# Kernel tuning notes

Measured on AMD Instinct MI355X. Metric: run time of the kernel, lower is better.

Reference implementation:

```python
import jax, jax.numpy as jnp
import numpy as np

D_MODEL = 1024
N_HEADS = 16
HEAD_DIM = D_MODEL // N_HEADS


def setup_inputs() -> dict:
    key = jax.random.key(0)
    ks = jax.random.split(key, 12)
    B, S = 1, 4096
    s = 1.0 / np.sqrt(D_MODEL)
    return {
        "query": jax.random.normal(ks[0], (B, S, D_MODEL), jnp.float32),
        "key": jax.random.normal(ks[1], (B, S, D_MODEL), jnp.float32),
        "value": jax.random.normal(ks[2], (B, S, D_MODEL), jnp.float32),
        "attention_mask": jnp.ones((B, S), jnp.int32),
        "Wq": jax.random.normal(ks[3], (D_MODEL, D_MODEL), jnp.float32) * s,
        "bq": jax.random.normal(ks[4], (D_MODEL,), jnp.float32) * s,
        "Wk": jax.random.normal(ks[5], (D_MODEL, D_MODEL), jnp.float32) * s,
        "bk": jax.random.normal(ks[6], (D_MODEL,), jnp.float32) * s,
        "Wv": jax.random.normal(ks[7], (D_MODEL, D_MODEL), jnp.float32) * s,
        "bv": jax.random.normal(ks[8], (D_MODEL,), jnp.float32) * s,
        "Wo": jax.random.normal(ks[9], (D_MODEL, D_MODEL), jnp.float32) * s,
        "bo": jax.random.normal(ks[10], (D_MODEL,), jnp.float32) * s,
    }


def reference(query, key, value, attention_mask, Wq, bq, Wk, bk, Wv, bv, Wo, bo):
    B = query.shape[0]

    def split_heads(x):  # [B,S,D] -> [B,H,S,Dh]
        return x.reshape(B, -1, N_HEADS, HEAD_DIM).transpose(0, 2, 1, 3)

    q = split_heads(query @ Wq + bq)
    k = split_heads(key @ Wk + bk)
    v = split_heads(value @ Wv + bv)

    scores = jnp.einsum("bhqd,bhkd->bhqk", q, k) / np.sqrt(HEAD_DIM)
    # 2D mask [B, Skv] -> [B,1,1,Skv]; 0 positions filled with -1e9
    mask = attention_mask[:, None, None, :]
    scores = jnp.where(mask == 0, jnp.float32(-1e9), scores)
    weights = jax.nn.softmax(scores, axis=-1)
    out = jnp.einsum("bhqk,bhkd->bhqd", weights, v)
    out = out.transpose(0, 2, 1, 3).reshape(B, -1, D_MODEL)
    return out @ Wo + bo
```

## Files before the change

### kernel.cpp

```cpp
#include <hip/hip_runtime.h>
#include <hip/hip_bf16.h>
#include <cstdint>

typedef __attribute__((ext_vector_type(8))) short short8;
typedef __attribute__((ext_vector_type(4))) float floatx4;
typedef unsigned short u16;

#define D_MODEL 1024
#define S_LEN 4096
#define N_HEADS 16
#define HEAD_DIM 64
#define SCALE_LOG2E 0.18033688f

__device__ __forceinline__ u16 f2bf(float x) {
    union { float f; uint32_t u; } v; v.f = x;
    uint32_t u = v.u;
    u += 0x7fffu + ((u >> 16) & 1u);
    return (u16)(u >> 16);
}

__device__ __forceinline__ void load_lds16(const u16* g, u16* l) {
    __builtin_amdgcn_global_load_lds(
        (const __attribute__((address_space(1))) uint32_t*)g,
        (__attribute__((address_space(3))) uint32_t*)l, 16, 0, 0);
}

#define PREP_CONV 12288
#define PREP_TR   4096
struct PrepArgs {
    const float* cs[3]; u16* cd[3];
    const float* ts[4]; u16* td[4]; float tscale[4];
    const int* mask; float* madd; int* clean;
};
__global__ __launch_bounds__(256) void prep(PrepArgs a) {
    __shared__ u16 tile[32][34];
    const int bx = blockIdx.x;
    const int tid = threadIdx.x;
    if (bx < PREP_CONV) {
        const int z = bx >> 12;
        const int i = (bx & 4095) * 256 + tid;
        float4 v = reinterpret_cast<const float4*>(a.cs[z])[i];
        ushort4 o;
        o.x = f2bf(v.x); o.y = f2bf(v.y); o.z = f2bf(v.z); o.w = f2bf(v.w);
        reinterpret_cast<ushort4*>(a.cd[z])[i] = o;
    } else if (bx < PREP_CONV + PREP_TR) {
        const int b = bx - PREP_CONV;
        const int z = b >> 10;
        const int t = b & 1023;
        const float* __restrict__ in = a.ts[z];
        u16* __restrict__ out = a.td[z];
        const float sc = a.tscale[z];
        const int c0 = (t & 31) * 32, r0 = (t >> 5) * 32;
        const int tx = tid & 31, ty = tid >> 5;
        #pragma unroll
        for (int j = 0; j < 32; j += 8)
            tile[ty + j][tx] = f2bf(in[(size_t)(r0 + ty + j) * D_MODEL + c0 + tx] * sc);
        __syncthreads();
        #pragma unroll
        for (int j = 0; j < 32; j += 8)
            out[(size_t)(c0 + ty + j) * D_MODEL + r0 + tx] = tile[tx][ty + j];
    } else {
        const int b = bx - PREP_CONV - PREP_TR;
        const int i = b * 256 + tid;
        const int v = a.mask[i];
        a.madd[i] = (v == 0) ? -1.0e30f : 0.f;
        const unsigned long long bal = __ballot(v != 0);
        if ((tid & 63) == 0) a.clean[b * 4 + (tid >> 6)] = (bal == ~0ull) ? 1 : 0;
    }
}

template <typename OutT>
__device__ __forceinline__ void gemm_bt_core(const u16* __restrict__ A, const u16* __restrict__ Bt,
                                             const float* __restrict__ bias, OutT* __restrict__ C,
                                             int M, int N, int K, int bx, int by, int trC,
                                             float bscale) {
    __shared__ u16 As[3][128 * 64];
    __shared__ u16 Bs[3][128 * 64];
    const int tid = threadIdx.x;
    const int wave = tid >> 6, lane = tid & 63;
    const int quad = lane >> 4, n16 = lane & 15;
    const int wm = wave >> 1, wn = wave & 1;
    const int m0 = by * 128, n0 = bx * 128;
    const int rl = lane >> 3, cl = lane & 7;
    const int stg_c = (cl ^ (rl & 7)) * 8;
    const int swz = n16 & 7;
    const int KI = K >> 6;

    floatx4 acc[4][4];
    #pragma unroll
    for (int i = 0; i < 4; ++i)
        #pragma unroll
        for (int t = 0; t < 4; ++t) acc[i][t] = (floatx4)0.f;

    #pragma unroll
    for (int p = 0; p < 2; ++p) {
        #pragma unroll
        for (int u = 0; u < 4; ++u) {
            const int r = wave * 32 + u * 8 + rl;
            load_lds16(&A[(size_t)(m0 + r) * K + p * 64 + stg_c], &As[p][(wave * 32 + u * 8) * 64]);
            load_lds16(&Bt[(size_t)(n0 + r) * K + p * 64 + stg_c], &Bs[p][(wave * 32 + u * 8) * 64]);
        }
    }

    int cur = 0;
    #pragma unroll 1
    for (int it = 0; it < KI; ++it) {
        asm volatile("s_waitcnt vmcnt(8)\n\ts_barrier" ::: "memory");
        const int nb = (cur >= 1) ? cur - 1 : 2;
        const int kn = ((it + 2) & (KI - 1)) * 64;
        #pragma unroll
        for (int u = 0; u < 4; ++u) {
            const int r = wave * 32 + u * 8 + rl;
            load_lds16(&A[(size_t)(m0 + r) * K + kn + stg_c], &As[nb][(wave * 32 + u * 8) * 64]);
            load_lds16(&Bt[(size_t)(n0 + r) * K + kn + stg_c], &Bs[nb][(wave * 32 + u * 8) * 64]);
        }
        #pragma unroll
        for (int kk = 0; kk < 2; ++kk) {
            const int sw = ((kk * 4 + quad) ^ swz) * 8;
            short8 a[4], b[4];
            #pragma unroll
            for (int i = 0; i < 4; ++i)
                a[i] = *reinterpret_cast<const short8*>(&As[cur][(wm * 64 + i * 16 + n16) * 64 + sw]);
            #pragma unroll
            for (int t = 0; t < 4; ++t)
                b[t] = *reinterpret_cast<const short8*>(&Bs[cur][(wn * 64 + t * 16 + n16) * 64 + sw]);
            #pragma unroll
            for (int i = 0; i < 4; ++i)
                #pragma unroll
                for (int t = 0; t < 4; ++t)
                    acc[i][t] = __builtin_amdgcn_mfma_f32_16x16x32_bf16(a[i], b[t], acc[i][t], 0, 0, 0);
        }
        cur = (cur >= 2) ? 0 : cur + 1;
    }
    asm volatile("s_waitcnt vmcnt(0)" ::: "memory");

    if (trC) {
        if constexpr (sizeof(OutT) == 2) {
            #pragma unroll
            for (int t = 0; t < 4; ++t) {
                const int col = n0 + wn * 64 + t * 16 + n16;
                const float bvs = bias[col] * bscale;
                #pragma unroll
                for (int i = 0; i < 4; ++i) {
                    const int row = m0 + wm * 64 + i * 16 + quad * 4;
                    ushort4 o;
                    o.x = f2bf(acc[i][t][0] + bvs);
                    o.y = f2bf(acc[i][t][1] + bvs);
                    o.z = f2bf(acc[i][t][2] + bvs);
                    o.w = f2bf(acc[i][t][3] + bvs);
                    *reinterpret_cast<ushort4*>(&C[(size_t)col * M + row]) = o;
                }
            }
        }
    } else {
        #pragma unroll
        for (int t = 0; t < 4; ++t) {
            const int col = n0 + wn * 64 + t * 16 + n16;
            const float bvs = bias[col] * bscale;
            #pragma unroll
            for (int i = 0; i < 4; ++i) {
                #pragma unroll
                for (int r = 0; r < 4; ++r) {
                    const int row = m0 + wm * 64 + i * 16 + quad * 4 + r;
                    const float val = acc[i][t][r] + bvs;
                    if constexpr (sizeof(OutT) == 2) C[(size_t)row * N + col] = f2bf(val);
                    else                             C[(size_t)row * N + col] = val;
                }
            }
        }
    }
}

struct QkvArgs {
    const u16* A[3]; const u16* B[3]; const float* bias[3]; u16* C[3]; float bscale[3];
};

__global__ __launch_bounds__(256) void gemm_qkv(QkvArgs args, int M, int N, int K) {
    const int z = blockIdx.z;
    gemm_bt_core<u16>(args.A[z], args.B[z], args.bias[z], args.C[z], M, N, K,
                      blockIdx.x, blockIdx.y, z == 2 ? 1 : 0, args.bscale[z]);
}

__global__ __launch_bounds__(256) void gemm_out(const u16* __restrict__ A, const u16* __restrict__ Bt,
                                                const float* __restrict__ bias, float* __restrict__ C,
                                                int M, int N, int K) {
    gemm_bt_core<float>(A, Bt, bias, C, M, N, K, blockIdx.x, blockIdx.y, 0, 1.0f);
}

__global__ __launch_bounds__(512) void flash_attn(const u16* __restrict__ Q, const u16* __restrict__ Kb,
                                                  const u16* __restrict__ Vt,
                                                  const float* __restrict__ madd,
                                                  const int* __restrict__ clean,
                                                  u16* __restrict__ O) {
    __shared__ u16 Ks[3 * 64 * 64];
    __shared__ u16 Vs[3 * 64 * 64];
    __shared__ u16 Ps[8][16 * 64];
    const int tid = threadIdx.x;
    const int wave = tid >> 6, lane = tid & 63;
    const int quad = lane >> 4, n16 = lane & 15;
    const int bid = blockIdx.x;
    const int h = (bid & 7) * 2 + ((bid >> 3) & 1);
    const int qt = bid >> 4;
    const int hd = h * HEAD_DIM;
    const int q0 = qt * 128 + wave * 16;

    const int rl = lane >> 3, cl = lane & 7;
    const int swz = n16 & 7;
    const int stg_row = wave * 8 + rl;
    const int stg_c = (cl ^ (rl & 7)) * 8;
    const int ldst = (wave * 8) * 64;

    short8 b_q[2];
    #pragma unroll
    for (int kk = 0; kk < 2; ++kk)
        b_q[kk] = *reinterpret_cast<const short8*>(
            &Q[(size_t)(q0 + n16) * D_MODEL + hd + kk * 32 + quad * 8]);

    short8 vone;
    #pragma unroll
    for (int i = 0; i < 8; ++i) vone[i] = (short)0x3F80;

    floatx4 o_acc[4];
    floatx4 l_acc = (floatx4)0.f;
    #pragma unroll
    for (int t = 0; t < 4; ++t) o_acc[t] = (floatx4)0.f;

    #pragma unroll
    for (int p = 0; p < 2; ++p) {
        load_lds16(&Kb[(size_t)(p * 64 + stg_row) * D_MODEL + hd + stg_c], &Ks[p * 4096 + ldst]);
        load_lds16(&Vt[(size_t)(hd + stg_row) * S_LEN + p * 64 + stg_c], &Vs[p * 4096 + ldst]);
    }

    int cur = 0;
    #pragma unroll 1
    for (int it = 0; it < 64; ++it) {
        asm volatile("s_waitcnt vmcnt(2)\n\ts_barrier" ::: "memory");

        const int nb = (cur >= 1) ? cur - 1 : 2;
        const int kn = ((it + 2) & 63) * 64;
        load_lds16(&Kb[(size_t)(kn + stg_row) * D_MODEL + hd + stg_c], &Ks[nb * 4096 + ldst]);
        load_lds16(&Vt[(size_t)(hd + stg_row) * S_LEN + kn + stg_c], &Vs[nb * 4096 + ldst]);

        const u16* KsC = &Ks[cur * 4096];
        const u16* VsC = &Vs[cur * 4096];

        floatx4 s[4];
        #pragma unroll
        for (int t = 0; t < 4; ++t) {
            s[t] = (floatx4)0.f;
            #pragma unroll
            for (int kk = 0; kk < 2; ++kk) {
                const int sw = ((kk * 4 + quad) ^ swz) * 8;
                short8 ak = *reinterpret_cast<const short8*>(&KsC[(t * 16 + n16) * 64 + sw]);
                s[t] = __builtin_amdgcn_mfma_f32_16x16x32_bf16(ak, b_q[kk], s[t], 0, 0, 0);
            }
        }
        if (clean[it]) {
            #pragma unroll
            for (int t = 0; t < 4; ++t) {
                const float p0 = __builtin_amdgcn_exp2f(s[t][0]);
                const float p1 = __builtin_amdgcn_exp2f(s[t][1]);
                const float p2 = __builtin_amdgcn_exp2f(s[t][2]);
                const float p3 = __builtin_amdgcn_exp2f(s[t][3]);
                union { __hip_bfloat162 h; uint32_t u; } pa, pb;
                pa.h = __float22bfloat162_rn(make_float2(p0, p1));
                pb.h = __float22bfloat162_rn(make_float2(p2, p3));
                uint2 w; w.x = pa.u; w.y = pb.u;
                const int cw = t * 2 + (quad >> 1);
                *reinterpret_cast<uint2*>(
                    &Ps[wave][n16 * 64 + ((cw ^ swz) * 8 + (quad & 1) * 4)]) = w;
            }
        } else {
            const int k0 = it * 64;
            #pragma unroll
            for (int t = 0; t < 4; ++t) {
                const float4 mv = *reinterpret_cast<const float4*>(&madd[k0 + t * 16 + quad * 4]);
                const float p0 = __builtin_amdgcn_exp2f(s[t][0] + mv.x);
                const float p1 = __builtin_amdgcn_exp2f(s[t][1] + mv.y);
                const float p2 = __builtin_amdgcn_exp2f(s[t][2] + mv.z);
                const float p3 = __builtin_amdgcn_exp2f(s[t][3] + mv.w);
                union { __hip_bfloat162 h; uint32_t u; } pa, pb;
                pa.h = __float22bfloat162_rn(make_float2(p0, p1));
                pb.h = __float22bfloat162_rn(make_float2(p2, p3));
                uint2 w; w.x = pa.u; w.y = pb.u;
                const int cw = t * 2 + (quad >> 1);
                *reinterpret_cast<uint2*>(
                    &Ps[wave][n16 * 64 + ((cw ^ swz) * 8 + (quad & 1) * 4)]) = w;
            }
        }
        asm volatile("s_waitcnt lgkmcnt(0)" ::: "memory");
        short8 ap[2];
        #pragma unroll
        for (int kkv = 0; kkv < 2; ++kkv)
            ap[kkv] = *reinterpret_cast<const short8*>(
                &Ps[wave][n16 * 64 + ((kkv * 4 + quad) ^ swz) * 8]);
        asm volatile("" ::: "memory");
        #pragma unroll
        for (int kkv = 0; kkv < 2; ++kkv) {
            l_acc = __builtin_amdgcn_mfma_f32_16x16x32_bf16(ap[kkv], vone, l_acc, 0, 0, 0);
            #pragma unroll
            for (int t = 0; t < 4; ++t) {
                const int sw = ((kkv * 4 + quad) ^ swz) * 8;
                short8 bv = *reinterpret_cast<const short8*>(&VsC[(t * 16 + n16) * 64 + sw]);
                o_acc[t] = __builtin_amdgcn_mfma_f32_16x16x32_bf16(ap[kkv], bv, o_acc[t], 0, 0, 0);
            }
        }
        cur = (cur >= 2) ? 0 : cur + 1;
    }
    asm volatile("s_waitcnt vmcnt(0)" ::: "memory");
    float lir[4];
    #pragma unroll
    for (int r = 0; r < 4; ++r) lir[r] = 1.f / l_acc[r];
    #pragma unroll
    for (int t = 0; t < 4; ++t)
        #pragma unroll
        for (int r = 0; r < 4; ++r)
            O[(size_t)(q0 + quad * 4 + r) * D_MODEL + hd + t * 16 + n16] =
                f2bf(o_acc[t][r] * lir[r]);
}

extern "C" void kernel_launch(void* const* d_in, const int* in_sizes, int n_in,
                              void* d_out, int out_size, void* d_ws, size_t ws_size,
                              hipStream_t stream) {
    const float* query = (const float*)d_in[0];
    const float* key   = (const float*)d_in[1];
    const float* value = (const float*)d_in[2];
    const int*   mask  = (const int*)d_in[3];
    const float* Wq = (const float*)d_in[4];
    const float* bq = (const float*)d_in[5];
    const float* Wk = (const float*)d_in[6];
    const float* bk = (const float*)d_in[7];
    const float* Wv = (const float*)d_in[8];
    const float* bv = (const float*)d_in[9];
    const float* Wo = (const float*)d_in[10];
    const float* bo = (const float*)d_in[11];
    float* out = (float*)d_out;

    char* ws = (char*)d_ws;
    const size_t SZ_SD = (size_t)S_LEN * D_MODEL * 2;
    const size_t SZ_W  = (size_t)D_MODEL * D_MODEL * 2;
    u16* qb  = (u16*)(ws);
    u16* kb  = (u16*)(ws + SZ_SD);
    u16* vb  = (u16*)(ws + 2 * SZ_SD);
    u16* Wqt = (u16*)(ws + 3 * SZ_SD);
    u16* Wkt = (u16*)(ws + 3 * SZ_SD + SZ_W);
    u16* Wvt = (u16*)(ws + 3 * SZ_SD + 2 * SZ_W);
    u16* Wot = (u16*)(ws + 3 * SZ_SD + 3 * SZ_W);
    u16* Qp  = (u16*)(ws + 3 * SZ_SD + 4 * SZ_W);
    u16* Kp  = (u16*)(ws + 4 * SZ_SD + 4 * SZ_W);
    u16* Vpt = (u16*)(ws + 5 * SZ_SD + 4 * SZ_W);
    float* maddf = (float*)(ws + 6 * SZ_SD + 4 * SZ_W);
    int* cleanf  = (int*)(ws + 6 * SZ_SD + 4 * SZ_W + S_LEN * sizeof(float));
    u16* Oa  = kb;

    PrepArgs pa;
    pa.cs[0] = query; pa.cs[1] = key; pa.cs[2] = value;
    pa.cd[0] = qb;    pa.cd[1] = kb;  pa.cd[2] = vb;
    pa.ts[0] = Wq; pa.ts[1] = Wk; pa.ts[2] = Wv; pa.ts[3] = Wo;
    pa.td[0] = Wqt; pa.td[1] = Wkt; pa.td[2] = Wvt; pa.td[3] = Wot;
    pa.tscale[0] = SCALE_LOG2E; pa.tscale[1] = 1.f; pa.tscale[2] = 1.f; pa.tscale[3] = 1.f;
    pa.mask = mask; pa.madd = maddf; pa.clean = cleanf;
    prep<<<dim3(PREP_CONV + PREP_TR + 16), 256, 0, stream>>>(pa);

    QkvArgs qa;
    qa.A[0] = qb;  qa.A[1] = kb;  qa.A[2] = vb;
    qa.B[0] = Wqt; qa.B[1] = Wkt; qa.B[2] = Wvt;
    qa.bias[0] = bq; qa.bias[1] = bk; qa.bias[2] = bv;
    qa.C[0] = Qp; qa.C[1] = Kp; qa.C[2] = Vpt;
    qa.bscale[0] = SCALE_LOG2E; qa.bscale[1] = 1.f; qa.bscale[2] = 1.f;
    gemm_qkv<<<dim3(8, 32, 3), 256, 0, stream>>>(qa, S_LEN, D_MODEL, D_MODEL);

    flash_attn<<<dim3(512), 512, 0, stream>>>(Qp, Kp, Vpt, maddf, cleanf, Oa);

    gemm_out<<<dim3(8, 32), 256, 0, stream>>>(Oa, Wot, bo, out, S_LEN, D_MODEL, D_MODEL);
}
```

Before: 294.2 us.

## Give each attention wave two query tiles and use smaller output-GEMM tiles

The flash attention kernel moves from 8 waves with 16 query rows each to 4 waves with 32 query rows each. Each K/V fragment read from LDS now feeds two MFMAs, which halves LDS reads per MFMA but raises register pressure and leaves fewer waves per block. The output projection gets its own 64x128 tile kernel with triple-buffered LDS and a 512-block grid, replacing the shared core, so more blocks are available to fill the CUs.

```diff
diff --git a/kernel.cpp b/kernel.cpp
--- a/kernel.cpp
+++ b/kernel.cpp
@@ -184,17 +184,97 @@
 __global__ __launch_bounds__(256) void gemm_out(const u16* __restrict__ A, const u16* __restrict__ Bt,
                                                 const float* __restrict__ bias, float* __restrict__ C,
                                                 int M, int N, int K) {
-    gemm_bt_core<float>(A, Bt, bias, C, M, N, K, blockIdx.x, blockIdx.y, 0, 1.0f);
-}
-
-__global__ __launch_bounds__(512) void flash_attn(const u16* __restrict__ Q, const u16* __restrict__ Kb,
+    __shared__ u16 As[3][64 * 64];
+    __shared__ u16 Bs[3][128 * 64];
+    const int tid = threadIdx.x;
+    const int wave = tid >> 6, lane = tid & 63;
+    const int quad = lane >> 4, n16 = lane & 15;
+    const int wm = wave >> 1, wn = wave & 1;
+    const int m0 = blockIdx.y * 64, n0 = blockIdx.x * 128;
+    const int rl = lane >> 3, cl = lane & 7;
+    const int stg_c = (cl ^ (rl & 7)) * 8;
+    const int swz = n16 & 7;
+    const int KI = K >> 6;
+
+    floatx4 acc[2][4];
+    #pragma unroll
+    for (int i = 0; i < 2; ++i)
+        #pragma unroll
+        for (int t = 0; t < 4; ++t) acc[i][t] = (floatx4)0.f;
+
+    #pragma unroll
+    for (int p = 0; p < 2; ++p) {
+        #pragma unroll
+        for (int u = 0; u < 2; ++u) {
+            const int r = wave * 16 + u * 8 + rl;
+            load_lds16(&A[(size_t)(m0 + r) * K + p * 64 + stg_c], &As[p][(wave * 16 + u * 8) * 64]);
+        }
+        #pragma unroll
+        for (int u = 0; u < 4; ++u) {
+            const int r = wave * 32 + u * 8 + rl;
+            load_lds16(&Bt[(size_t)(n0 + r) * K + p * 64 + stg_c], &Bs[p][(wave * 32 + u * 8) * 64]);
+        }
+    }
+
+    int cur = 0;
+    #pragma unroll 1
+    for (int it = 0; it < KI; ++it) {
+        asm volatile("s_waitcnt vmcnt(6)\n\ts_barrier" ::: "memory");
+        const int nb = (cur >= 1) ? cur - 1 : 2;
+        const int kn = ((it + 2) & (KI - 1)) * 64;
+        #pragma unroll
+        for (int u = 0; u < 2; ++u) {
+            const int r = wave * 16 + u * 8 + rl;
+            load_lds16(&A[(size_t)(m0 + r) * K + kn + stg_c], &As[nb][(wave * 16 + u * 8) * 64]);
+        }
+        #pragma unroll
+        for (int u = 0; u < 4; ++u) {
+            const int r = wave * 32 + u * 8 + rl;
+            load_lds16(&Bt[(size_t)(n0 + r) * K + kn + stg_c], &Bs[nb][(wave * 32 + u * 8) * 64]);
+        }
+        #pragma unroll
+        for (int kk = 0; kk < 2; ++kk) {
+            const int sw = ((kk * 4 + quad) ^ swz) * 8;
+            short8 a[2], b[4];
+            #pragma unroll
+            for (int i = 0; i < 2; ++i)
+                a[i] = *reinterpret_cast<const short8*>(&As[cur][(wm * 32 + i * 16 + n16) * 64 + sw]);
+            #pragma unroll
+            for (int t = 0; t < 4; ++t)
+                b[t] = *reinterpret_cast<const short8*>(&Bs[cur][(wn * 64 + t * 16 + n16) * 64 + sw]);
+            #pragma unroll
+            for (int i = 0; i < 2; ++i)
+                #pragma unroll
+                for (int t = 0; t < 4; ++t)
+                    acc[i][t] = __builtin_amdgcn_mfma_f32_16x16x32_bf16(a[i], b[t], acc[i][t], 0, 0, 0);
+        }
+        cur = (cur >= 2) ? 0 : cur + 1;
+    }
+    asm volatile("s_waitcnt vmcnt(0)" ::: "memory");
+
+    #pragma unroll
+    for (int t = 0; t < 4; ++t) {
+        const int col = n0 + wn * 64 + t * 16 + n16;
+        const float bvs = bias[col];
+        #pragma unroll
+        for (int i = 0; i < 2; ++i) {
+            #pragma unroll
+            for (int r = 0; r < 4; ++r) {
+                const int row = m0 + wm * 32 + i * 16 + quad * 4 + r;
+                C[(size_t)row * N + col] = acc[i][t][r] + bvs;
+            }
+        }
+    }
+}
+
+__global__ __launch_bounds__(256) void flash_attn(const u16* __restrict__ Q, const u16* __restrict__ Kb,
                                                   const u16* __restrict__ Vt,
                                                   const float* __restrict__ madd,
                                                   const int* __restrict__ clean,
                                                   u16* __restrict__ O) {
-    __shared__ u16 Ks[3 * 64 * 64];
-    __shared__ u16 Vs[3 * 64 * 64];
-    __shared__ u16 Ps[8][16 * 64];
+    __shared__ u16 Ks[3 * 4096];
+    __shared__ u16 Vs[3 * 4096];
+    __shared__ u16 Ps[4][32 * 64];
     const int tid = threadIdx.x;
     const int wave = tid >> 6, lane = tid & 63;
     const int quad = lane >> 4, n16 = lane & 15;
@@ -202,121 +282,153 @@
     const int h = (bid & 7) * 2 + ((bid >> 3) & 1);
     const int qt = bid >> 4;
     const int hd = h * HEAD_DIM;
-    const int q0 = qt * 128 + wave * 16;
+    const int q0 = qt * 128 + wave * 32;
 
     const int rl = lane >> 3, cl = lane & 7;
     const int swz = n16 & 7;
-    const int stg_row = wave * 8 + rl;
     const int stg_c = (cl ^ (rl & 7)) * 8;
-    const int ldst = (wave * 8) * 64;
-
-    short8 b_q[2];
-    #pragma unroll
-    for (int kk = 0; kk < 2; ++kk)
-        b_q[kk] = *reinterpret_cast<const short8*>(
-            &Q[(size_t)(q0 + n16) * D_MODEL + hd + kk * 32 + quad * 8]);
+
+    short8 b_q[2][2];
+    #pragma unroll
+    for (int qi = 0; qi < 2; ++qi)
+        #pragma unroll
+        for (int kk = 0; kk < 2; ++kk)
+            b_q[qi][kk] = *reinterpret_cast<const short8*>(
+                &Q[(size_t)(q0 + qi * 16 + n16) * D_MODEL + hd + kk * 32 + quad * 8]);
 
     short8 vone;
     #pragma unroll
     for (int i = 0; i < 8; ++i) vone[i] = (short)0x3F80;
 
-    floatx4 o_acc[4];
-    floatx4 l_acc = (floatx4)0.f;
-    #pragma unroll
-    for (int t = 0; t < 4; ++t) o_acc[t] = (floatx4)0.f;
+    floatx4 o_acc[2][4];
+    floatx4 l_acc[2];
+    #pragma unroll
+    for (int qi = 0; qi < 2; ++qi) {
+        l_acc[qi] = (floatx4)0.f;
+        #pragma unroll
+        for (int t = 0; t < 4; ++t) o_acc[qi][t] = (floatx4)0.f;
+    }
 
     #pragma unroll
     for (int p = 0; p < 2; ++p) {
-        load_lds16(&Kb[(size_t)(p * 64 + stg_row) * D_MODEL + hd + stg_c], &Ks[p * 4096 + ldst]);
-        load_lds16(&Vt[(size_t)(hd + stg_row) * S_LEN + p * 64 + stg_c], &Vs[p * 4096 + ldst]);
+        #pragma unroll
+        for (int u = 0; u < 2; ++u) {
+            const int r = wave * 16 + u * 8 + rl;
+            load_lds16(&Kb[(size_t)(p * 64 + r) * D_MODEL + hd + stg_c], &Ks[p * 4096 + (wave * 16 + u * 8) * 64]);
+            load_lds16(&Vt[(size_t)(hd + r) * S_LEN + p * 64 + stg_c], &Vs[p * 4096 + (wave * 16 + u * 8) * 64]);
+        }
     }
 
     int cur = 0;
     #pragma unroll 1
     for (int it = 0; it < 64; ++it) {
-        asm volatile("s_waitcnt vmcnt(2)\n\ts_barrier" ::: "memory");
+        asm volatile("s_waitcnt vmcnt(4)\n\ts_barrier" ::: "memory");
 
         const int nb = (cur >= 1) ? cur - 1 : 2;
         const int kn = ((it + 2) & 63) * 64;
-        load_lds16(&Kb[(size_t)(kn + stg_row) * D_MODEL + hd + stg_c], &Ks[nb * 4096 + ldst]);
-        load_lds16(&Vt[(size_t)(hd + stg_row) * S_LEN + kn + stg_c], &Vs[nb * 4096 + ldst]);
+        #pragma unroll
+        for (int u = 0; u < 2; ++u) {
+            const int r = wave * 16 + u * 8 + rl;
+            load_lds16(&Kb[(size_t)(kn + r) * D_MODEL + hd + stg_c], &Ks[nb * 4096 + (wave * 16 + u * 8) * 64]);
+            load_lds16(&Vt[(size_t)(hd + r) * S_LEN + kn + stg_c], &Vs[nb * 4096 + (wave * 16 + u * 8) * 64]);
+        }
 
         const u16* KsC = &Ks[cur * 4096];
         const u16* VsC = &Vs[cur * 4096];
 
-        floatx4 s[4];
+        floatx4 s[4][2];
         #pragma unroll
         for (int t = 0; t < 4; ++t) {
-            s[t] = (floatx4)0.f;
+            #pragma unroll
+            for (int qi = 0; qi < 2; ++qi) s[t][qi] = (floatx4)0.f;
             #pragma unroll
             for (int kk = 0; kk < 2; ++kk) {
                 const int sw = ((kk * 4 + quad) ^ swz) * 8;
                 short8 ak = *reinterpret_cast<const short8*>(&KsC[(t * 16 + n16) * 64 + sw]);
-                s[t] = __builtin_amdgcn_mfma_f32_16x16x32_bf16(ak, b_q[kk], s[t], 0, 0, 0);
+                #pragma unroll
+                for (int qi = 0; qi < 2; ++qi)
+                    s[t][qi] = __builtin_amdgcn_mfma_f32_16x16x32_bf16(ak, b_q[qi][kk], s[t][qi], 0, 0, 0);
             }
         }
         if (clean[it]) {
             #pragma unroll
             for (int t = 0; t < 4; ++t) {
-                const float p0 = __builtin_amdgcn_exp2f(s[t][0]);
-                const float p1 = __builtin_amdgcn_exp2f(s[t][1]);
-                const float p2 = __builtin_amdgcn_exp2f(s[t][2]);
-                const float p3 = __builtin_amdgcn_exp2f(s[t][3]);
-                union { __hip_bfloat162 h; uint32_t u; } pa, pb;
-                pa.h = __float22bfloat162_rn(make_float2(p0, p1));
-                pb.h = __float22bfloat162_rn(make_float2(p2, p3));
-                uint2 w; w.x = pa.u; w.y = pb.u;
-                const int cw = t * 2 + (quad >> 1);
-                *reinterpret_cast<uint2*>(
-                    &Ps[wave][n16 * 64 + ((cw ^ swz) * 8 + (quad & 1) * 4)]) = w;
+                #pragma unroll
+                for (int qi = 0; qi < 2; ++qi) {
+                    const float p0 = __builtin_amdgcn_exp2f(s[t][qi][0]);
+                    const float p1 = __builtin_amdgcn_exp2f(s[t][qi][1]);
+                    const float p2 = __builtin_amdgcn_exp2f(s[t][qi][2]);
+                    const float p3 = __builtin_amdgcn_exp2f(s[t][qi][3]);
+                    union { __hip_bfloat162 h; uint32_t u; } pa, pb;
+                    pa.h = __float22bfloat162_rn(make_float2(p0, p1));
+                    pb.h = __float22bfloat162_rn(make_float2(p2, p3));
+                    uint2 w; w.x = pa.u; w.y = pb.u;
+                    const int cw = t * 2 + (quad >> 1);
+                    *reinterpret_cast<uint2*>(
+                        &Ps[wave][(qi * 16 + n16) * 64 + ((cw ^ swz) * 8 + (quad & 1) * 4)]) = w;
+                }
             }
         } else {
             const int k0 = it * 64;
             #pragma unroll
             for (int t = 0; t < 4; ++t) {
                 const float4 mv = *reinterpret_cast<const float4*>(&madd[k0 + t * 16 + quad * 4]);
-                const float p0 = __builtin_amdgcn_exp2f(s[t][0] + mv.x);
-                const float p1 = __builtin_amdgcn_exp2f(s[t][1] + mv.y);
-                const float p2 = __builtin_amdgcn_exp2f(s[t][2] + mv.z);
-                const float p3 = __builtin_amdgcn_exp2f(s[t][3] + mv.w);
-                union { __hip_bfloat162 h; uint32_t u; } pa, pb;
-                pa.h = __float22bfloat162_rn(make_float2(p0, p1));
-                pb.h = __float22bfloat162_rn(make_float2(p2, p3));
-                uint2 w; w.x = pa.u; w.y = pb.u;
-                const int cw = t * 2 + (quad >> 1);
-                *reinterpret_cast<uint2*>(
-                    &Ps[wave][n16 * 64 + ((cw ^ swz) * 8 + (quad & 1) * 4)]) = w;
+                #pragma unroll
+                for (int qi = 0; qi < 2; ++qi) {
+                    const float p0 = __builtin_amdgcn_exp2f(s[t][qi][0] + mv.x);
+                    const float p1 = __builtin_amdgcn_exp2f(s[t][qi][1] + mv.y);
+                    const float p2 = __builtin_amdgcn_exp2f(s[t][qi][2] + mv.z);
+                    const float p3 = __builtin_amdgcn_exp2f(s[t][qi][3] + mv.w);
+                    union { __hip_bfloat162 h; uint32_t u; } pa, pb;
+                    pa.h = __float22bfloat162_rn(make_float2(p0, p1));
+                    pb.h = __float22bfloat162_rn(make_float2(p2, p3));
+                    uint2 w; w.x = pa.u; w.y = pb.u;
+                    const int cw = t * 2 + (quad >> 1);
+                    *reinterpret_cast<uint2*>(
+                        &Ps[wave][(qi * 16 + n16) * 64 + ((cw ^ swz) * 8 + (quad & 1) * 4)]) = w;
+                }
             }
         }
         asm volatile("s_waitcnt lgkmcnt(0)" ::: "memory");
-        short8 ap[2];
+        short8 ap[2][2];
+        #pragma unroll
+        for (int qi = 0; qi < 2; ++qi)
+            #pragma unroll
+            for (int kkv = 0; kkv < 2; ++kkv)
+                ap[qi][kkv] = *reinterpret_cast<const short8*>(
+                    &Ps[wave][(qi * 16 + n16) * 64 + ((kkv * 4 + quad) ^ swz) * 8]);
+        asm volatile("" ::: "memory");
         #pragma unroll
         for (int kkv = 0; kkv < 2; ++kkv)
-            ap[kkv] = *reinterpret_cast<const short8*>(
-                &Ps[wave][n16 * 64 + ((kkv * 4 + quad) ^ swz) * 8]);
-        asm volatile("" ::: "memory");
-        #pragma unroll
-        for (int kkv = 0; kkv < 2; ++kkv) {
-            l_acc = __builtin_amdgcn_mfma_f32_16x16x32_bf16(ap[kkv], vone, l_acc, 0, 0, 0);
-            #pragma unroll
-            for (int t = 0; t < 4; ++t) {
+            #pragma unroll
+            for (int qi = 0; qi < 2; ++qi)
+                l_acc[qi] = __builtin_amdgcn_mfma_f32_16x16x32_bf16(ap[qi][kkv], vone, l_acc[qi], 0, 0, 0);
+        #pragma unroll
+        for (int t = 0; t < 4; ++t) {
+            #pragma unroll
+            for (int kkv = 0; kkv < 2; ++kkv) {
                 const int sw = ((kkv * 4 + quad) ^ swz) * 8;
                 short8 bv = *reinterpret_cast<const short8*>(&VsC[(t * 16 + n16) * 64 + sw]);
-                o_acc[t] = __builtin_amdgcn_mfma_f32_16x16x32_bf16(ap[kkv], bv, o_acc[t], 0, 0, 0);
+                #pragma unroll
+                for (int qi = 0; qi < 2; ++qi)
+                    o_acc[qi][t] = __builtin_amdgcn_mfma_f32_16x16x32_bf16(ap[qi][kkv], bv, o_acc[qi][t], 0, 0, 0);
             }
         }
         cur = (cur >= 2) ? 0 : cur + 1;
     }
     asm volatile("s_waitcnt vmcnt(0)" ::: "memory");
-    float lir[4];
-    #pragma unroll
-    for (int r = 0; r < 4; ++r) lir[r] = 1.f / l_acc[r];
-    #pragma unroll
-    for (int t = 0; t < 4; ++t)
-        #pragma unroll
-        for (int r = 0; r < 4; ++r)
-            O[(size_t)(q0 + quad * 4 + r) * D_MODEL + hd + t * 16 + n16] =
-                f2bf(o_acc[t][r] * lir[r]);
+    #pragma unroll
+    for (int qi = 0; qi < 2; ++qi) {
+        float lir[4];
+        #pragma unroll
+        for (int r = 0; r < 4; ++r) lir[r] = 1.f / l_acc[qi][r];
+        #pragma unroll
+        for (int t = 0; t < 4; ++t)
+            #pragma unroll
+            for (int r = 0; r < 4; ++r)
+                O[(size_t)(q0 + qi * 16 + quad * 4 + r) * D_MODEL + hd + t * 16 + n16] =
+                    f2bf(o_acc[qi][t][r] * lir[r]);
+    }
 }
 
 extern "C" void kernel_launch(void* const* d_in, const int* in_sizes, int n_in,
@@ -370,7 +482,7 @@
     qa.bscale[0] = SCALE_LOG2E; qa.bscale[1] = 1.f; qa.bscale[2] = 1.f;
     gemm_qkv<<<dim3(8, 32, 3), 256, 0, stream>>>(qa, S_LEN, D_MODEL, D_MODEL);
 
-    flash_attn<<<dim3(512), 512, 0, stream>>>(Qp, Kp, Vpt, maddf, cleanf, Oa);
-
-    gemm_out<<<dim3(8, 32), 256, 0, stream>>>(Oa, Wot, bo, out, S_LEN, D_MODEL, D_MODEL);
-}
+    flash_attn<<<dim3(512), 256, 0, stream>>>(Qp, Kp, Vpt, maddf, cleanf, Oa);
+
+    gemm_out<<<dim3(8, 64), 256, 0, stream>>>(Oa, Wot, bo, out, S_LEN, D_MODEL, D_MODEL);
+}
```

Result: faster. 284.5 us (-3.3%).
